# Kernel optimization log

Hardware: AMD Instinct MI355X
Metric: run time of the kernel (lower is better)

The kernel has to match this reference:

```python
import jax, jax.numpy as jnp
import numpy as np

N = 50000      # nodes
E = 500000     # edges
H = 128        # hidden_channels
P = 1024       # number of (src,dst) link pairs: z==1 and z==2 counts
L = 3          # num_layers
MAXZ = 1000


def setup_inputs() -> dict:
    key = jax.random.key(0)
    ks = jax.random.split(key, 16)
    # z: P src nodes (label 1), P dst nodes (label 2), rest random labels >= 3
    z = jnp.concatenate([
        jnp.ones((P,), jnp.int32),
        jnp.full((P,), 2, jnp.int32),
        jax.random.randint(ks[0], (N - 2 * P,), 3, MAXZ, dtype=jnp.int32),
    ])
    edge_index = jax.random.randint(ks[1], (2, E), 0, N, dtype=jnp.int32)
    batch = jnp.zeros((N,), jnp.int32)  # unused in executed branch
    s = 1.0 / np.sqrt(H)
    z_table = jax.random.normal(ks[2], (MAXZ, H), jnp.float32) * 0.1
    conv_Wl = jax.random.normal(ks[3], (L, H, H), jnp.float32) * s
    conv_bl = jax.random.normal(ks[4], (L, H), jnp.float32) * 0.01
    conv_Wr = jax.random.normal(ks[5], (L, H, H), jnp.float32) * s
    W0 = jax.random.normal(ks[6], (H, H), jnp.float32) * s
    b0 = jax.random.normal(ks[7], (H,), jnp.float32) * 0.01
    W1 = jax.random.normal(ks[8], (H, H), jnp.float32) * s
    b1 = jax.random.normal(ks[9], (H,), jnp.float32) * 0.01
    W2 = jax.random.normal(ks[10], (1, H), jnp.float32) * s
    b2 = jax.random.normal(ks[11], (1,), jnp.float32) * 0.01
    return dict(z=z, edge_index=edge_index, batch=batch, z_table=z_table,
                conv_Wl=conv_Wl, conv_bl=conv_bl, conv_Wr=conv_Wr,
                W0=W0, b0=b0, W1=W1, b1=b1, W2=W2, b2=b2)


def _sage_conv(x, Wl, bl, Wr, src, dst):
    # x: [2, N, H]; mean-aggregate neighbor messages then linear (PyG SAGEConv)
    msgs = x[:, src, :]  # [2, E, H] gather
    agg = jax.vmap(lambda m: jax.ops.segment_sum(m, dst, num_segments=N))(msgs)
    deg = jax.ops.segment_sum(jnp.ones((dst.shape[0],), x.dtype), dst, num_segments=N)
    agg = agg / jnp.maximum(deg, 1.0)[None, :, None]
    return agg @ Wl.T + bl + x @ Wr.T  # lin_l(mean) + bias + lin_r(x)


def reference(z, edge_index, batch, z_table, conv_Wl, conv_bl, conv_Wr,
              W0, b0, W1, b1, W2, b2):
    src, dst = edge_index[0], edge_index[1]
    # ([[1],[2]] == z).long() -> [2, N] in {0,1}; embed -> [2, N, H]
    lbl = (jnp.arange(1, 3, dtype=z.dtype)[:, None] == z[None, :]).astype(jnp.int32)
    x = z_table[lbl]
    for i in range(L - 1):
        x = jax.nn.relu(_sage_conv(x, conv_Wl[i], conv_bl[i], conv_Wr[i], src, dst))
    x = _sage_conv(x, conv_Wl[L - 1], conv_bl[L - 1], conv_Wr[L - 1], src, dst)
    h = jax.nn.relu(x @ W0.T + b0).sum(axis=0)  # [N, H]
    src_idx = jnp.nonzero(z == 1, size=P)[0]
    dst_idx = jnp.nonzero(z == 2, size=P)[0]
    p = h[src_idx] * h[dst_idx]                 # [P, H]
    return jax.nn.relu(p @ W1.T + b1) @ W2.T + b2  # [P, 1]
```

## Files before the change

### kernel.cpp

```cpp
#include <hip/hip_runtime.h>
#include <stdint.h>

#define HH 128
typedef unsigned long long ull;
typedef unsigned short u16;

__device__ __forceinline__ ull shfl_up64(ull v, int d) {
  unsigned lo = (unsigned)__shfl_up((int)(unsigned)(v & 0xffffffffULL), d);
  unsigned hi = (unsigned)__shfl_up((int)(unsigned)(v >> 32), d);
  return ((ull)hi << 32) | (ull)lo;
}
__device__ __forceinline__ ull shfl_down64(ull v, int d) {
  unsigned lo = (unsigned)__shfl_down((int)(unsigned)(v & 0xffffffffULL), d);
  unsigned hi = (unsigned)__shfl_down((int)(unsigned)(v >> 32), d);
  return ((ull)hi << 32) | (ull)lo;
}

__global__ __launch_bounds__(256) void k_ytab(
    const float* __restrict__ zt, const float* __restrict__ Wl0,
    const float* __restrict__ Wr0, const float* __restrict__ Wl2,
    const float* __restrict__ Wr2, const float* __restrict__ bl0,
    const float* __restrict__ bl1, const float* __restrict__ Wl3,
    const float* __restrict__ Wr3, const float* __restrict__ W0,
    const float* __restrict__ bl2, const float* __restrict__ b0,
    float* __restrict__ y_l, float* __restrict__ y_rb,
    float* __restrict__ vecs_g, float* __restrict__ Wcl,
    float* __restrict__ Wcr, float* __restrict__ b03,
    const int* __restrict__ z, int N, ull* __restrict__ cnt64,
    int* __restrict__ mark, int* __restrict__ status, int* __restrict__ bctr) {
  __shared__ float ztS[2][HH];
  __shared__ float vS[4][HH];
  __shared__ float xS[16][HH];
  __shared__ float wAS[32][HH + 1], wBS[32][HH + 1];
  int t = threadIdx.x;
  {
    int gid = blockIdx.x * 256 + t;
    int nthr = gridDim.x * 256;
    for (int n = gid; n < N; n += nthr) {
      cnt64[n] = 0ULL;
      mark[n] = (z[n] <= 2) ? 1 : 0;
    }
    if (gid < 64) status[gid] = 0;
    if (gid == 0) *bctr = 0;
  }
  ztS[t >> 7][t & 127] = zt[t];
  __syncthreads();
  int j = t & 127, half = t >> 7;
  int jw = t >> 3, kk0 = (t & 7) * 4;
  float accA = 0.f, accR = 0.f;
  for (int kt = 0; kt < 4; kt++) {
    __syncthreads();
#pragma unroll
    for (int q = 0; q < 4; q++) {
      int jj = q * 32 + jw;
      float4 va = *(const float4*)(Wl0 + (size_t)jj * HH + kt * 32 + kk0);
      float4 vb = *(const float4*)(Wr0 + (size_t)jj * HH + kt * 32 + kk0);
      wAS[kk0 + 0][jj] = va.x; wAS[kk0 + 1][jj] = va.y;
      wAS[kk0 + 2][jj] = va.z; wAS[kk0 + 3][jj] = va.w;
      wBS[kk0 + 0][jj] = vb.x; wBS[kk0 + 1][jj] = vb.y;
      wBS[kk0 + 2][jj] = vb.z; wBS[kk0 + 3][jj] = vb.w;
    }
    __syncthreads();
#pragma unroll
    for (int kk = 0; kk < 32; kk++) {
      float zk = ztS[half][kt * 32 + kk];
      accA = fmaf(zk, wAS[kk][j], accA);
      accR = fmaf(zk, wBS[kk][j], accR);
    }
  }
  __syncthreads();
  vS[half][j] = accA;
  vS[2 + half][j] = accR;
  __syncthreads();
  if (blockIdx.x == 0) {
    vecs_g[t] = vS[t >> 7][t & 127];
    vecs_g[256 + t] = vS[2 + (t >> 7)][t & 127];
  }
  int v0 = blockIdx.x * 16;
#pragma unroll
  for (int rep = 0; rep < 8; rep++) {
    int idx = t + rep * 256;
    int r = idx >> 7, jx = idx & 127;
    int v = v0 + r;
    int d = v >> 4, cnt = (v >> 1) & 7, sel = v & 1;
    float invd = 1.0f / (float)max(d, 1);
    float u1 = (float)cnt * invd, u0 = (float)(d - cnt) * invd;
    xS[r][jx] = fmaxf(fmaf(u0, vS[0][jx], fmaf(u1, vS[1][jx], bl0[jx] + vS[2 + sel][jx])), 0.f);
  }
  int rh = t >> 7;
  float al[8], ar[8];
#pragma unroll
  for (int q = 0; q < 8; q++) { al[q] = 0.f; ar[q] = 0.f; }
  for (int kt = 0; kt < 4; kt++) {
    __syncthreads();
#pragma unroll
    for (int q = 0; q < 4; q++) {
      int jj = q * 32 + jw;
      float4 va = *(const float4*)(Wl2 + (size_t)jj * HH + kt * 32 + kk0);
      float4 vb = *(const float4*)(Wr2 + (size_t)jj * HH + kt * 32 + kk0);
      wAS[kk0 + 0][jj] = va.x; wAS[kk0 + 1][jj] = va.y;
      wAS[kk0 + 2][jj] = va.z; wAS[kk0 + 3][jj] = va.w;
      wBS[kk0 + 0][jj] = vb.x; wBS[kk0 + 1][jj] = vb.y;
      wBS[kk0 + 2][jj] = vb.z; wBS[kk0 + 3][jj] = vb.w;
    }
    __syncthreads();
#pragma unroll
    for (int kk = 0; kk < 32; kk++) {
      float wl = wAS[kk][j], wr = wBS[kk][j];
#pragma unroll
      for (int q = 0; q < 8; q++) {
        float x = xS[rh * 8 + q][kt * 32 + kk];
        al[q] = fmaf(x, wl, al[q]);
        ar[q] = fmaf(x, wr, ar[q]);
      }
    }
  }
  float bb = bl1[j];
#pragma unroll
  for (int q = 0; q < 8; q++) {
    int v = v0 + rh * 8 + q;
    y_l[((size_t)v << 7) + j] = al[q];
    y_rb[((size_t)v << 7) + j] = ar[q] + bb;
  }
  if (blockIdx.x < 32) {
    __syncthreads();
    const float* Wsrc = (blockIdx.x < 16) ? Wl3 : Wr3;
    float* Wdst = (blockIdx.x < 16) ? Wcl : Wcr;
    int j0 = (blockIdx.x & 15) * 8;
    {
      float4 w0v = *(const float4*)(W0 + (size_t)j0 * HH + t * 4);
      int r = (t * 4) >> 7, m = (t * 4) & 127;
      xS[r][m] = w0v.x; xS[r][m + 1] = w0v.y; xS[r][m + 2] = w0v.z; xS[r][m + 3] = w0v.w;
    }
    __syncthreads();
    int k = t & 127, h = t >> 7;
    float acc[4] = {0.f, 0.f, 0.f, 0.f};
    for (int m = 0; m < HH; m++) {
      float v = Wsrc[(size_t)m * HH + k];
#pragma unroll
      for (int r = 0; r < 4; r++) acc[r] = fmaf(xS[h * 4 + r][m], v, acc[r]);
    }
#pragma unroll
    for (int r = 0; r < 4; r++) Wdst[(size_t)(j0 + h * 4 + r) * HH + k] = acc[r];
  } else if (blockIdx.x == 32) {
    __syncthreads();
    if (t < HH) vS[0][t] = bl2[t];
    float acc = 0.f;
    for (int kt = 0; kt < 4; kt++) {
      __syncthreads();
#pragma unroll
      for (int q = 0; q < 4; q++) {
        int jj = q * 32 + jw;
        float4 v0 = *(const float4*)(W0 + (size_t)jj * HH + kt * 32 + kk0);
        wAS[kk0 + 0][jj] = v0.x; wAS[kk0 + 1][jj] = v0.y;
        wAS[kk0 + 2][jj] = v0.z; wAS[kk0 + 3][jj] = v0.w;
      }
      __syncthreads();
#pragma unroll
      for (int kk = 0; kk < 32; kk++)
        acc = fmaf(vS[0][kt * 32 + kk], wAS[kk][j], acc);
    }
    if (t < HH) b03[j] = acc + b0[j];
  }
}

__global__ void k_edge(const int* __restrict__ z, const int* __restrict__ src,
                       const int* __restrict__ dst, int E,
                       ull* __restrict__ cnt64, int* __restrict__ mark,
                       int* __restrict__ pos) {
  int e = blockIdx.x * blockDim.x + threadIdx.x;
  if (e >= E) return;
  int s = src[e], d = dst[e];
  int zs = z[s];
  ull val = 1ULL | ((ull)(zs == 1) << 20) | ((ull)(zs == 2) << 40);
  ull old = atomicAdd(&cnt64[d], val);
  pos[e] = (int)(old & 0xFFFFF);
  if (z[d] <= 2) mark[s] = 1;
}

__global__ __launch_bounds__(256) void k_scanpost(
    const ull* __restrict__ cnt64, const int* __restrict__ mark,
    const int* __restrict__ z, int N, int P,
    int* __restrict__ rowptr, int* __restrict__ mlist, int* __restrict__ minv,
    int* __restrict__ plist, int* __restrict__ Rm, int4* __restrict__ pack,
    u16* __restrict__ keyN, int* __restrict__ bctr,
    ull* __restrict__ aggbuf, int* __restrict__ status) {
  __shared__ ull wsum[4];
  __shared__ int chunk_s;
  __shared__ ull excl_s;
  int t = threadIdx.x;
  if (t == 0) chunk_s = atomicAdd(bctr, 1);
  __syncthreads();
  int b = chunk_s;
  int base = b * 1024 + t * 4;
  ull l[4]; ull s = 0;
#pragma unroll
  for (int i = 0; i < 4; i++) {
    int idx = base + i; ull v = 0;
    if (idx < N) {
      int zz = z[idx];
      v = (cnt64[idx] & 0xFFFFFULL) | ((ull)mark[idx] << 20)
        | ((ull)(zz == 1) << 40) | ((ull)(zz == 2) << 52);
    }
    l[i] = s; s += v;
  }
  int lane = t & 63, wid = t >> 6;
  ull vi = s;
  for (int d2 = 1; d2 < 64; d2 <<= 1) { ull o = shfl_up64(vi, d2); if (lane >= d2) vi += o; }
  if (lane == 63) wsum[wid] = vi;
  __syncthreads();
  ull woff = 0;
  for (int w = 0; w < wid; w++) woff += wsum[w];
  ull thrbase = woff + vi - s;
  if (t == 0) {
    ull btot = wsum[0] + wsum[1] + wsum[2] + wsum[3];
    __hip_atomic_store(&aggbuf[b], btot, __ATOMIC_RELAXED, __HIP_MEMORY_SCOPE_AGENT);
    __hip_atomic_store(&status[b], 1, __ATOMIC_RELEASE, __HIP_MEMORY_SCOPE_AGENT);
  }
  if (t < 64) {
    ull excl = 0;
    for (int p = lane; p < b; p += 64) {
      while (__hip_atomic_load(&status[p], __ATOMIC_ACQUIRE, __HIP_MEMORY_SCOPE_AGENT) == 0)
        __builtin_amdgcn_s_sleep(1);
      excl += __hip_atomic_load(&aggbuf[p], __ATOMIC_RELAXED, __HIP_MEMORY_SCOPE_AGENT);
    }
    for (int o = 32; o > 0; o >>= 1) excl += shfl_down64(excl, o);
    if (lane == 0) excl_s = excl;
  }
  __syncthreads();
  ull blockbase = excl_s;
#pragma unroll
  for (int i = 0; i < 4; i++) {
    int idx = base + i;
    if (idx >= N) break;
    ull sf = blockbase + thrbase + l[i];
    int rp = (int)(sf & 0xFFFFF);
    int mp = (int)((sf >> 20) & 0xFFFFF);
    int r1 = (int)((sf >> 40) & 0xFFF);
    int r2 = (int)(sf >> 52);
    rowptr[idx] = rp;
    int mk = mark[idx];
    if (mk) { mlist[mp] = idx; minv[idx] = mp; }
    int zz = z[idx];
    if (zz == 1) plist[r1] = idx;
    else if (zz == 2) plist[P + r2] = idx;
    ull cv = cnt64[idx];
    int dd = (int)(cv & 0xFFFFF), c1 = (int)((cv >> 20) & 0xFFFFF), c2 = (int)((cv >> 40) & 0xFFFFF);
    pack[idx] = make_int4(dd, c1, c2, zz);
    int wcls = (zz == 1) ? 1 : ((zz == 2) ? 2 : 0);
    u16 key;
    if (dd < 64 && c1 < 8 && c2 < 8) key = (u16)(dd | (c1 << 6) | (c2 << 9) | (wcls << 12));
    else key = 0x8000;
    keyN[idx] = key;
    if (idx == N - 1) *Rm = mp + mk;
  }
}

__global__ void k_csrk(const int* __restrict__ src, const int* __restrict__ dst, int E,
                       const int* __restrict__ rowptr, const int* __restrict__ pos,
                       const u16* __restrict__ keyN, const int* __restrict__ mark,
                       ull* __restrict__ csrk) {
  int e = blockIdx.x * blockDim.x + threadIdx.x;
  if (e >= E) return;
  int d = dst[e];
  if (!mark[d]) return;
  int s = src[e];
  csrk[rowptr[d] + pos[e]] = (ull)(unsigned)s | ((ull)keyN[s] << 32);
}

__device__ __noinline__ float4 yrow_fb(const float* __restrict__ vecs,
    const float* __restrict__ bl0, const float* __restrict__ Wm,
    int j4, int d, int cnt, int sel) {
  float invd = 1.0f / (float)max(d, 1);
  float u1 = (float)cnt * invd, u0 = (float)(d - cnt) * invd;
  const float* Rv = vecs + (2 + sel) * HH;
  float4 acc = make_float4(0, 0, 0, 0);
  for (int k = 0; k < HH; k++) {
    float x = fmaxf(fmaf(u0, vecs[k], fmaf(u1, vecs[HH + k], bl0[k] + Rv[k])), 0.f);
    acc.x = fmaf(x, Wm[(j4 + 0) * HH + k], acc.x);
    acc.y = fmaf(x, Wm[(j4 + 1) * HH + k], acc.y);
    acc.z = fmaf(x, Wm[(j4 + 2) * HH + k], acc.z);
    acc.w = fmaf(x, Wm[(j4 + 3) * HH + k], acc.w);
  }
  return acc;
}

__device__ __forceinline__ float4 yl_fetch(ull cv, int ch, int chsel, int j4,
    const float* __restrict__ y_l, const int4* __restrict__ pack,
    const float* __restrict__ vecs, const float* __restrict__ bl0,
    const float* __restrict__ Wl2) {
  int key = (int)(cv >> 32);
  if (key & 0x8000) {
    int s = (int)(cv & 0xFFFFFFFFULL);
    int4 p = pack[s];
    int cc = ch ? p.z : p.y;
    int sel = (p.w == chsel) ? 1 : 0;
    return yrow_fb(vecs, bl0, Wl2, j4, p.x, cc, sel);
  }
  int cc = (key >> (6 + 3 * ch)) & 7;
  int sel = (((key >> 12) & 3) == chsel) ? 1 : 0;
  int row = ((key & 63) << 4) + (cc << 1) + sel;
  return *(const float4*)(y_l + ((size_t)row << 7) + j4);
}

__global__ __launch_bounds__(256) void k_agg2Y(const int4* __restrict__ pack,
    const ull* __restrict__ csrk, const float* __restrict__ y_l,
    const float* __restrict__ y_rb, const float* __restrict__ vecs,
    const float* __restrict__ bl0, const float* __restrict__ bl1,
    const float* __restrict__ Wl2, const float* __restrict__ Wr2,
    const int* __restrict__ rowptr, const int* __restrict__ mlist,
    const int* __restrict__ Rdev, float* __restrict__ x2c) {
  int gt = blockIdx.x * blockDim.x + threadIdx.x;
  int w = gt >> 6, lane = gt & 63;
  int nw = (gridDim.x * blockDim.x) >> 6;
  int T = *Rdev;
  int ch = lane >> 5, j4 = (lane & 31) * 4;
  int chsel = ch + 1;
  for (int task = w; task < T; task += nw) {
    int n = mlist[task];
    int4 pn = pack[n];
    int beg = rowptr[n], d = pn.x;
    float4 acc = make_float4(0, 0, 0, 0);
    int i = 0;
    for (; i + 4 <= d; i += 4) {
      ull c0 = csrk[beg + i], c1 = csrk[beg + i + 1];
      ull c2 = csrk[beg + i + 2], c3 = csrk[beg + i + 3];
      float4 v0 = yl_fetch(c0, ch, chsel, j4, y_l, pack, vecs, bl0, Wl2);
      float4 v1 = yl_fetch(c1, ch, chsel, j4, y_l, pack, vecs, bl0, Wl2);
      float4 v2 = yl_fetch(c2, ch, chsel, j4, y_l, pack, vecs, bl0, Wl2);
      float4 v3 = yl_fetch(c3, ch, chsel, j4, y_l, pack, vecs, bl0, Wl2);
      acc.x += v0.x + v1.x + v2.x + v3.x;
      acc.y += v0.y + v1.y + v2.y + v3.y;
      acc.z += v0.z + v1.z + v2.z + v3.z;
      acc.w += v0.w + v1.w + v2.w + v3.w;
    }
    for (; i < d; i++) {
      float4 v0 = yl_fetch(csrk[beg + i], ch, chsel, j4, y_l, pack, vecs, bl0, Wl2);
      acc.x += v0.x; acc.y += v0.y; acc.z += v0.z; acc.w += v0.w;
    }
    float inv = 1.0f / (float)max(d, 1);
    int ccn = ch ? pn.z : pn.y;
    int seln = (pn.w == chsel) ? 1 : 0;
    float4 yr;
    if (pn.x < 64 && ccn < 8) {
      yr = *(const float4*)(y_rb + ((size_t)(((pn.x << 3) + ccn) * 2 + seln) << 7) + j4);
    } else {
      yr = yrow_fb(vecs, bl0, Wr2, j4, pn.x, ccn, seln);
      yr.x += bl1[j4]; yr.y += bl1[j4 + 1]; yr.z += bl1[j4 + 2]; yr.w += bl1[j4 + 3];
    }
    float4 o;
    o.x = fmaxf(fmaf(acc.x, inv, yr.x), 0.f);
    o.y = fmaxf(fmaf(acc.y, inv, yr.y), 0.f);
    o.z = fmaxf(fmaf(acc.z, inv, yr.z), 0.f);
    o.w = fmaxf(fmaf(acc.w, inv, yr.w), 0.f);
    *(float4*)(x2c + (size_t)task * 256 + ch * HH + j4) = o;
  }
}

__global__ __launch_bounds__(256) void k_agg3(const float* __restrict__ x2c,
    const ull* __restrict__ csrk, const int* __restrict__ rowptr,
    const int4* __restrict__ pack, const int* __restrict__ plist,
    const int* __restrict__ minv, int T, float* __restrict__ aggp) {
  int gt = blockIdx.x * blockDim.x + threadIdx.x;
  int w = gt >> 6, lane = gt & 63;
  int nw = (gridDim.x * blockDim.x) >> 6;
  int j4 = lane * 4;
  for (int task = w; task < T; task += nw) {
    int n = plist[task];
    int beg = rowptr[n], d = pack[n].x;
    float4 acc = make_float4(0, 0, 0, 0);
    int i = 0;
    for (; i + 4 <= d; i += 4) {
      int m0 = minv[(int)(csrk[beg + i] & 0xFFFFFFFFULL)];
      int m1 = minv[(int)(csrk[beg + i + 1] & 0xFFFFFFFFULL)];
      int m2 = minv[(int)(csrk[beg + i + 2] & 0xFFFFFFFFULL)];
      int m3 = minv[(int)(csrk[beg + i + 3] & 0xFFFFFFFFULL)];
      float4 v0 = *(const float4*)(x2c + (size_t)m0 * 256 + j4);
      float4 v1 = *(const float4*)(x2c + (size_t)m1 * 256 + j4);
      float4 v2 = *(const float4*)(x2c + (size_t)m2 * 256 + j4);
      float4 v3 = *(const float4*)(x2c + (size_t)m3 * 256 + j4);
      acc.x += v0.x + v1.x + v2.x + v3.x;
      acc.y += v0.y + v1.y + v2.y + v3.y;
      acc.z += v0.z + v1.z + v2.z + v3.z;
      acc.w += v0.w + v1.w + v2.w + v3.w;
    }
    for (; i < d; i++) {
      int m0 = minv[(int)(csrk[beg + i] & 0xFFFFFFFFULL)];
      float4 v0 = *(const float4*)(x2c + (size_t)m0 * 256 + j4);
      acc.x += v0.x; acc.y += v0.y; acc.z += v0.z; acc.w += v0.w;
    }
    float inv = 1.0f / (float)max(d, 1);
    float4 o = make_float4(acc.x * inv, acc.y * inv, acc.z * inv, acc.w * inv);
    *(float4*)(aggp + (size_t)task * 256 + j4) = o;
  }
}

__global__ __launch_bounds__(256) void k_tail(const float* __restrict__ aggp,
    const float* __restrict__ x2c, const float* __restrict__ Wcl,
    const float* __restrict__ Wcr, const float* __restrict__ b03,
    const float* __restrict__ W1, const float* __restrict__ b1,
    const float* __restrict__ W2, const float* __restrict__ b2,
    const int* __restrict__ plist, const int* __restrict__ minv,
    int P, float* __restrict__ out) {
  __shared__ float wAS[32][HH + 1], wBS[32][HH + 1];
  __shared__ float aS[2][256], xS[2][256], hS[2][256];
  __shared__ float pS[HH];
  __shared__ float wred[2];
  int t = threadIdx.x;
  int i0 = blockIdx.x;
  int tsk[2] = { i0, P + i0 };
  int j = t & 127, c = t >> 7;
#pragma unroll
  for (int g = 0; g < 2; g++) {
    int i = tsk[g];
    aS[g][t] = aggp[(size_t)i * 256 + t];
    xS[g][t] = x2c[(size_t)minv[plist[i]] * 256 + t];
  }
  float bias = b03[j];
  float acc0 = bias, acc1 = bias;
  int jw = t >> 3, kk0 = (t & 7) * 4;
  for (int kt = 0; kt < 4; kt++) {
    __syncthreads();
#pragma unroll
    for (int q = 0; q < 4; q++) {
      int jj = q * 32 + jw;
      float4 va = *(const float4*)(Wcl + (size_t)jj * HH + kt * 32 + kk0);
      float4 vb = *(const float4*)(Wcr + (size_t)jj * HH + kt * 32 + kk0);
      wAS[kk0 + 0][jj] = va.x; wAS[kk0 + 1][jj] = va.y;
      wAS[kk0 + 2][jj] = va.z; wAS[kk0 + 3][jj] = va.w;
      wBS[kk0 + 0][jj] = vb.x; wBS[kk0 + 1][jj] = vb.y;
      wBS[kk0 + 2][jj] = vb.z; wBS[kk0 + 3][jj] = vb.w;
    }
    __syncthreads();
#pragma unroll
    for (int kk = 0; kk < 32; kk++) {
      int k = kt * 32 + kk;
      float wl = wAS[kk][j], wr = wBS[kk][j];
      acc0 = fmaf(aS[0][c * HH + k], wl, fmaf(xS[0][c * HH + k], wr, acc0));
      acc1 = fmaf(aS[1][c * HH + k], wl, fmaf(xS[1][c * HH + k], wr, acc1));
    }
  }
  hS[0][t] = fmaxf(acc0, 0.f);
  hS[1][t] = fmaxf(acc1, 0.f);
  __syncthreads();
  if (t < HH)
    pS[t] = (hS[0][t] + hS[0][HH + t]) * (hS[1][t] + hS[1][HH + t]);
  float acc3 = b1[j];
  for (int kt = 0; kt < 4; kt++) {
    __syncthreads();
#pragma unroll
    for (int q = 0; q < 4; q++) {
      int jj = q * 32 + jw;
      float4 v = *(const float4*)(W1 + (size_t)jj * HH + kt * 32 + kk0);
      wAS[kk0 + 0][jj] = v.x; wAS[kk0 + 1][jj] = v.y;
      wAS[kk0 + 2][jj] = v.z; wAS[kk0 + 3][jj] = v.w;
    }
    __syncthreads();
#pragma unroll
    for (int kk = 0; kk < 32; kk++)
      acc3 = fmaf(pS[kt * 32 + kk], wAS[kk][j], acc3);
  }
  float v = fmaxf(acc3, 0.f) * W2[j];
  int lane = t & 63, wid = t >> 6;
  for (int off = 32; off > 0; off >>= 1) v += __shfl_down(v, off);
  if (wid < 2 && lane == 0) wred[wid] = v;
  __syncthreads();
  if (t == 0) out[i0] = wred[0] + wred[1] + b2[0];
}

extern "C" void kernel_launch(void* const* d_in, const int* in_sizes, int n_in,
                              void* d_out, int out_size, void* d_ws, size_t ws_size,
                              hipStream_t stream) {
  const int* z = (const int*)d_in[0];
  const int* ei = (const int*)d_in[1];
  const float* z_table = (const float*)d_in[3];
  const float* conv_Wl = (const float*)d_in[4];
  const float* conv_bl = (const float*)d_in[5];
  const float* conv_Wr = (const float*)d_in[6];
  const float* W0 = (const float*)d_in[7];
  const float* b0 = (const float*)d_in[8];
  const float* W1 = (const float*)d_in[9];
  const float* b1 = (const float*)d_in[10];
  const float* W2 = (const float*)d_in[11];
  const float* b2 = (const float*)d_in[12];
  float* out = (float*)d_out;

  int N = in_sizes[0];
  int E = in_sizes[1] / 2;
  int P = out_size;
  int P2 = 2 * P;
  const int* srcA = ei;
  const int* dstA = ei + E;

  char* basep = (char*)d_ws;
  size_t off = 0;
  auto alloc = [&](size_t bytes) -> char* {
    off = (off + 255) & ~(size_t)255;
    char* pp = basep + off; off += bytes; return pp;
  };
  float* y_l   = (float*)alloc((size_t)1024 * HH * 4);
  float* y_rb  = (float*)alloc((size_t)1024 * HH * 4);
  float* vecs  = (float*)alloc((size_t)4 * HH * 4);
  float* Wcl   = (float*)alloc((size_t)HH * HH * 4);
  float* Wcr   = (float*)alloc((size_t)HH * HH * 4);
  float* b03   = (float*)alloc((size_t)HH * 4);
  float* x2c   = (float*)alloc((size_t)N * 256 * 4);
  float* aggp  = (float*)alloc((size_t)P2 * 256 * 4);
  ull*   cnt64 = (ull*)alloc((size_t)N * 8);
  int*   mark  = (int*)alloc((size_t)N * 4);
  int*   pos   = (int*)alloc((size_t)E * 4);
  int*   rowptr= (int*)alloc((size_t)N * 4);
  int*   mlist = (int*)alloc((size_t)N * 4);
  int*   minv  = (int*)alloc((size_t)N * 4);
  int*   plist = (int*)alloc((size_t)P2 * 4);
  ull*   csrk  = (ull*)alloc((size_t)E * 8);
  ull*   aggbuf= (ull*)alloc(64 * 8);
  int*   status= (int*)alloc(64 * 4);
  int*   bctr  = (int*)alloc(256);
  int*   Rm_dev= (int*)alloc(256);
  u16*   keyN  = (u16*)alloc((size_t)N * 2);
  int4*  pack  = (int4*)alloc((size_t)N * 16);
  (void)ws_size; (void)n_in;

  k_ytab<<<64, 256, 0, stream>>>(z_table, conv_Wl, conv_Wr,
                                 conv_Wl + HH * HH, conv_Wr + HH * HH,
                                 conv_bl, conv_bl + HH,
                                 conv_Wl + 2 * HH * HH, conv_Wr + 2 * HH * HH,
                                 W0, conv_bl + 2 * HH, b0,
                                 y_l, y_rb, vecs, Wcl, Wcr, b03,
                                 z, N, cnt64, mark, status, bctr);
  k_edge<<<(E + 255) / 256, 256, 0, stream>>>(z, srcA, dstA, E, cnt64, mark, pos);
  int nb = (N + 1023) / 1024;
  k_scanpost<<<nb, 256, 0, stream>>>(cnt64, mark, z, N, P, rowptr, mlist, minv,
                                     plist, Rm_dev, pack, keyN, bctr, aggbuf, status);
  k_csrk<<<(E + 255) / 256, 256, 0, stream>>>(srcA, dstA, E, rowptr, pos, keyN, mark, csrk);
  k_agg2Y<<<2048, 256, 0, stream>>>(pack, csrk, y_l, y_rb, vecs, conv_bl, conv_bl + HH,
                                    conv_Wl + HH * HH, conv_Wr + HH * HH,
                                    rowptr, mlist, Rm_dev, x2c);
  k_agg3<<<512, 256, 0, stream>>>(x2c, csrk, rowptr, pack, plist, minv, P2, aggp);
  k_tail<<<P, 256, 0, stream>>>(aggp, x2c, Wcl, Wcr, b03, W1, b1, W2, b2,
                                plist, minv, P, out);
}
```

Measured before the change: 129.3 us.

## Split prep kernel into specialized block roles across a wider grid

The first kernel used to run on 64 blocks that each did the init loop, the ytab GEMM and, for some blocks, the weight-combination GEMMs in sequence. It now launches 257 blocks with separate roles: 64 for the y table, 32 for the Wl3/Wr3 times W0 products, one for the bias, and 160 that only initialize counters and marks. The weight product now stages Wsrc tiles in shared memory with float4 loads instead of strided scalar global reads. This shortens the critical path of the prep stage by spreading independent work across more CUs, at the cost of a larger launch.

New measurement: 122.7 us. 5.1% less time.

```diff
diff --git a/kernel.cpp b/kernel.cpp
--- a/kernel.cpp
+++ b/kernel.cpp
@@ -16,7 +16,7 @@
   return ((ull)hi << 32) | (ull)lo;
 }
 
-__global__ __launch_bounds__(256) void k_ytab(
+__global__ __launch_bounds__(256) void k_prep(
     const float* __restrict__ zt, const float* __restrict__ Wl0,
     const float* __restrict__ Wr0, const float* __restrict__ Wl2,
     const float* __restrict__ Wr2, const float* __restrict__ bl0,
@@ -33,117 +33,144 @@
   __shared__ float xS[16][HH];
   __shared__ float wAS[32][HH + 1], wBS[32][HH + 1];
   int t = threadIdx.x;
-  {
-    int gid = blockIdx.x * 256 + t;
-    int nthr = gridDim.x * 256;
-    for (int n = gid; n < N; n += nthr) {
+  int b = blockIdx.x;
+  int j = t & 127, half = t >> 7;
+  int jw = t >> 3, kk0 = (t & 7) * 4;
+
+  if (b >= 97) {
+    int local = (b - 97) * 256 + t;
+    int stride = 160 * 256;
+    for (int n = local; n < N; n += stride) {
       cnt64[n] = 0ULL;
       mark[n] = (z[n] <= 2) ? 1 : 0;
     }
-    if (gid < 64) status[gid] = 0;
-    if (gid == 0) *bctr = 0;
-  }
-  ztS[t >> 7][t & 127] = zt[t];
-  __syncthreads();
-  int j = t & 127, half = t >> 7;
-  int jw = t >> 3, kk0 = (t & 7) * 4;
-  float accA = 0.f, accR = 0.f;
-  for (int kt = 0; kt < 4; kt++) {
-    __syncthreads();
-#pragma unroll
-    for (int q = 0; q < 4; q++) {
-      int jj = q * 32 + jw;
-      float4 va = *(const float4*)(Wl0 + (size_t)jj * HH + kt * 32 + kk0);
-      float4 vb = *(const float4*)(Wr0 + (size_t)jj * HH + kt * 32 + kk0);
-      wAS[kk0 + 0][jj] = va.x; wAS[kk0 + 1][jj] = va.y;
-      wAS[kk0 + 2][jj] = va.z; wAS[kk0 + 3][jj] = va.w;
-      wBS[kk0 + 0][jj] = vb.x; wBS[kk0 + 1][jj] = vb.y;
-      wBS[kk0 + 2][jj] = vb.z; wBS[kk0 + 3][jj] = vb.w;
-    }
-    __syncthreads();
-#pragma unroll
-    for (int kk = 0; kk < 32; kk++) {
-      float zk = ztS[half][kt * 32 + kk];
-      accA = fmaf(zk, wAS[kk][j], accA);
-      accR = fmaf(zk, wBS[kk][j], accR);
-    }
-  }
-  __syncthreads();
-  vS[half][j] = accA;
-  vS[2 + half][j] = accR;
-  __syncthreads();
-  if (blockIdx.x == 0) {
-    vecs_g[t] = vS[t >> 7][t & 127];
-    vecs_g[256 + t] = vS[2 + (t >> 7)][t & 127];
-  }
-  int v0 = blockIdx.x * 16;
-#pragma unroll
-  for (int rep = 0; rep < 8; rep++) {
-    int idx = t + rep * 256;
-    int r = idx >> 7, jx = idx & 127;
-    int v = v0 + r;
-    int d = v >> 4, cnt = (v >> 1) & 7, sel = v & 1;
-    float invd = 1.0f / (float)max(d, 1);
-    float u1 = (float)cnt * invd, u0 = (float)(d - cnt) * invd;
-    xS[r][jx] = fmaxf(fmaf(u0, vS[0][jx], fmaf(u1, vS[1][jx], bl0[jx] + vS[2 + sel][jx])), 0.f);
-  }
-  int rh = t >> 7;
-  float al[8], ar[8];
-#pragma unroll
-  for (int q = 0; q < 8; q++) { al[q] = 0.f; ar[q] = 0.f; }
-  for (int kt = 0; kt < 4; kt++) {
-    __syncthreads();
-#pragma unroll
-    for (int q = 0; q < 4; q++) {
-      int jj = q * 32 + jw;
-      float4 va = *(const float4*)(Wl2 + (size_t)jj * HH + kt * 32 + kk0);
-      float4 vb = *(const float4*)(Wr2 + (size_t)jj * HH + kt * 32 + kk0);
-      wAS[kk0 + 0][jj] = va.x; wAS[kk0 + 1][jj] = va.y;
-      wAS[kk0 + 2][jj] = va.z; wAS[kk0 + 3][jj] = va.w;
-      wBS[kk0 + 0][jj] = vb.x; wBS[kk0 + 1][jj] = vb.y;
-      wBS[kk0 + 2][jj] = vb.z; wBS[kk0 + 3][jj] = vb.w;
-    }
-    __syncthreads();
-#pragma unroll
-    for (int kk = 0; kk < 32; kk++) {
-      float wl = wAS[kk][j], wr = wBS[kk][j];
-#pragma unroll
-      for (int q = 0; q < 8; q++) {
-        float x = xS[rh * 8 + q][kt * 32 + kk];
-        al[q] = fmaf(x, wl, al[q]);
-        ar[q] = fmaf(x, wr, ar[q]);
-      }
-    }
-  }
-  float bb = bl1[j];
-#pragma unroll
-  for (int q = 0; q < 8; q++) {
-    int v = v0 + rh * 8 + q;
-    y_l[((size_t)v << 7) + j] = al[q];
-    y_rb[((size_t)v << 7) + j] = ar[q] + bb;
-  }
-  if (blockIdx.x < 32) {
-    __syncthreads();
-    const float* Wsrc = (blockIdx.x < 16) ? Wl3 : Wr3;
-    float* Wdst = (blockIdx.x < 16) ? Wcl : Wcr;
-    int j0 = (blockIdx.x & 15) * 8;
+    if (b == 97) {
+      if (t < 64) status[t] = 0;
+      if (t == 0) *bctr = 0;
+    }
+    return;
+  }
+
+  if (b < 64) {
+    ztS[half][j] = zt[t];
+    __syncthreads();
+    float accA = 0.f, accR = 0.f;
+    for (int kt = 0; kt < 4; kt++) {
+      __syncthreads();
+#pragma unroll
+      for (int q = 0; q < 4; q++) {
+        int jj = q * 32 + jw;
+        float4 va = *(const float4*)(Wl0 + (size_t)jj * HH + kt * 32 + kk0);
+        float4 vb = *(const float4*)(Wr0 + (size_t)jj * HH + kt * 32 + kk0);
+        wAS[kk0 + 0][jj] = va.x; wAS[kk0 + 1][jj] = va.y;
+        wAS[kk0 + 2][jj] = va.z; wAS[kk0 + 3][jj] = va.w;
+        wBS[kk0 + 0][jj] = vb.x; wBS[kk0 + 1][jj] = vb.y;
+        wBS[kk0 + 2][jj] = vb.z; wBS[kk0 + 3][jj] = vb.w;
+      }
+      __syncthreads();
+#pragma unroll
+      for (int kk = 0; kk < 32; kk++) {
+        float zk = ztS[half][kt * 32 + kk];
+        accA = fmaf(zk, wAS[kk][j], accA);
+        accR = fmaf(zk, wBS[kk][j], accR);
+      }
+    }
+    __syncthreads();
+    vS[half][j] = accA;
+    vS[2 + half][j] = accR;
+    __syncthreads();
+    if (b == 0) {
+      vecs_g[t] = vS[t >> 7][t & 127];
+      vecs_g[256 + t] = vS[2 + (t >> 7)][t & 127];
+    }
+    int v0 = b * 16;
+#pragma unroll
+    for (int rep = 0; rep < 8; rep++) {
+      int idx = t + rep * 256;
+      int r = idx >> 7, jx = idx & 127;
+      int v = v0 + r;
+      int d = v >> 4, cnt = (v >> 1) & 7, sel = v & 1;
+      float invd = 1.0f / (float)max(d, 1);
+      float u1 = (float)cnt * invd, u0 = (float)(d - cnt) * invd;
+      xS[r][jx] = fmaxf(fmaf(u0, vS[0][jx], fmaf(u1, vS[1][jx], bl0[jx] + vS[2 + sel][jx])), 0.f);
+    }
+    int rh = half;
+    float al[8], ar[8];
+#pragma unroll
+    for (int q = 0; q < 8; q++) { al[q] = 0.f; ar[q] = 0.f; }
+    for (int kt = 0; kt < 4; kt++) {
+      __syncthreads();
+#pragma unroll
+      for (int q = 0; q < 4; q++) {
+        int jj = q * 32 + jw;
+        float4 va = *(const float4*)(Wl2 + (size_t)jj * HH + kt * 32 + kk0);
+        float4 vb = *(const float4*)(Wr2 + (size_t)jj * HH + kt * 32 + kk0);
+        wAS[kk0 + 0][jj] = va.x; wAS[kk0 + 1][jj] = va.y;
+        wAS[kk0 + 2][jj] = va.z; wAS[kk0 + 3][jj] = va.w;
+        wBS[kk0 + 0][jj] = vb.x; wBS[kk0 + 1][jj] = vb.y;
+        wBS[kk0 + 2][jj] = vb.z; wBS[kk0 + 3][jj] = vb.w;
+      }
+      __syncthreads();
+#pragma unroll
+      for (int kk = 0; kk < 32; kk++) {
+        float wl = wAS[kk][j], wr = wBS[kk][j];
+#pragma unroll
+        for (int q = 0; q < 8; q++) {
+          float x = xS[rh * 8 + q][kt * 32 + kk];
+          al[q] = fmaf(x, wl, al[q]);
+          ar[q] = fmaf(x, wr, ar[q]);
+        }
+      }
+    }
+    float bb = bl1[j];
+#pragma unroll
+    for (int q = 0; q < 8; q++) {
+      int v = v0 + rh * 8 + q;
+      y_l[((size_t)v << 7) + j] = al[q];
+      y_rb[((size_t)v << 7) + j] = ar[q] + bb;
+    }
+    return;
+  }
+
+  if (b < 96) {
+    int bb = b - 64;
+    const float* Wsrc = (bb < 16) ? Wl3 : Wr3;
+    float* Wdst = (bb < 16) ? Wcl : Wcr;
+    int j0 = (bb & 15) * 8;
     {
-      float4 w0v = *(const float4*)(W0 + (size_t)j0 * HH + t * 4);
+      float4 v = *(const float4*)(W0 + (size_t)j0 * HH + t * 4);
       int r = (t * 4) >> 7, m = (t * 4) & 127;
-      xS[r][m] = w0v.x; xS[r][m + 1] = w0v.y; xS[r][m + 2] = w0v.z; xS[r][m + 3] = w0v.w;
-    }
-    __syncthreads();
-    int k = t & 127, h = t >> 7;
+      xS[r][m] = v.x; xS[r][m + 1] = v.y; xS[r][m + 2] = v.z; xS[r][m + 3] = v.w;
+    }
+    int k = t & 127, h = half;
     float acc[4] = {0.f, 0.f, 0.f, 0.f};
-    for (int m = 0; m < HH; m++) {
-      float v = Wsrc[(size_t)m * HH + k];
-#pragma unroll
-      for (int r = 0; r < 4; r++) acc[r] = fmaf(xS[h * 4 + r][m], v, acc[r]);
-    }
-#pragma unroll
-    for (int r = 0; r < 4; r++) Wdst[(size_t)(j0 + h * 4 + r) * HH + k] = acc[r];
-  } else if (blockIdx.x == 32) {
-    __syncthreads();
+    for (int mt = 0; mt < 4; mt++) {
+      __syncthreads();
+#pragma unroll
+      for (int q = 0; q < 4; q++) {
+        int fl = t * 4 + q * 1024;
+        int mm = fl >> 7, kx = fl & 127;
+        float4 v = *(const float4*)(Wsrc + (size_t)(mt * 32 + mm) * HH + kx);
+        wAS[mm][kx] = v.x; wAS[mm][kx + 1] = v.y;
+        wAS[mm][kx + 2] = v.z; wAS[mm][kx + 3] = v.w;
+      }
+      __syncthreads();
+#pragma unroll
+      for (int mm = 0; mm < 32; mm++) {
+        float wv = wAS[mm][k];
+        int m = mt * 32 + mm;
+#pragma unroll
+        for (int r = 0; r < 4; r++)
+          acc[r] = fmaf(xS[h * 4 + r][m], wv, acc[r]);
+      }
+    }
+#pragma unroll
+    for (int r = 0; r < 4; r++)
+      Wdst[(size_t)(j0 + h * 4 + r) * HH + k] = acc[r];
+    return;
+  }
+
+  {
     if (t < HH) vS[0][t] = bl2[t];
     float acc = 0.f;
     for (int kt = 0; kt < 4; kt++) {
@@ -522,13 +549,13 @@
   int4*  pack  = (int4*)alloc((size_t)N * 16);
   (void)ws_size; (void)n_in;
 
-  k_ytab<<<64, 256, 0, stream>>>(z_table, conv_Wl, conv_Wr,
-                                 conv_Wl + HH * HH, conv_Wr + HH * HH,
-                                 conv_bl, conv_bl + HH,
-                                 conv_Wl + 2 * HH * HH, conv_Wr + 2 * HH * HH,
-                                 W0, conv_bl + 2 * HH, b0,
-                                 y_l, y_rb, vecs, Wcl, Wcr, b03,
-                                 z, N, cnt64, mark, status, bctr);
+  k_prep<<<257, 256, 0, stream>>>(z_table, conv_Wl, conv_Wr,
+                                  conv_Wl + HH * HH, conv_Wr + HH * HH,
+                                  conv_bl, conv_bl + HH,
+                                  conv_Wl + 2 * HH * HH, conv_Wr + 2 * HH * HH,
+                                  W0, conv_bl + 2 * HH, b0,
+                                  y_l, y_rb, vecs, Wcl, Wcr, b03,
+                                  z, N, cnt64, mark, status, bctr);
   k_edge<<<(E + 255) / 256, 256, 0, stream>>>(z, srcA, dstA, E, cnt64, mark, pos);
   int nb = (N + 1023) / 1024;
   k_scanpost<<<nb, 256, 0, stream>>>(cnt64, mark, z, N, P, rowptr, mlist, minv,
```
